# Kernel optimization log

Measured on AMD Instinct MI355X. Metric: run time of the kernel, lower is better.

The kernel has to match this reference:

```python
import jax, jax.numpy as jnp
import numpy as np

N, E, D = 50000, 1200000, 64
NEG_SLOPE = 0.2  # PyG GATConv LeakyReLU slope
EPS_SM = 1e-16   # PyG softmax eps
EPS_LN = 1e-5


def _glorot(key, shape):
    fan = shape[0]
    return jax.random.normal(key, shape, jnp.float32) / np.float32(np.sqrt(fan))


def setup_inputs() -> dict:
    key = jax.random.key(0)
    ks = jax.random.split(key, 16)
    inp = {
        "x": jax.random.normal(ks[0], (N, D), jnp.float32),
        "edge_index": jax.random.randint(ks[1], (2, E), 0, N, dtype=jnp.int32),
        # layer 0: bipartite-style (-1,-1) GATConv -> separate src/dst projections
        "W_src0": _glorot(ks[2], (D, D)), "W_dst0": _glorot(ks[3], (D, D)),
        "a_src0": _glorot(ks[4], (D,)), "a_dst0": _glorot(ks[5], (D,)),
        "b0": jnp.zeros((D,), jnp.float32),
        "lin_W0": _glorot(ks[6], (D, D)), "lin_b0": jnp.zeros((D,), jnp.float32),
        # layers 1,2: int in_channels -> shared projection for src and dst
        "W1": _glorot(ks[7], (D, D)),
        "a_src1": _glorot(ks[8], (D,)), "a_dst1": _glorot(ks[9], (D,)),
        "b1": jnp.zeros((D,), jnp.float32),
        "lin_W1": _glorot(ks[10], (D, D)), "lin_b1": jnp.zeros((D,), jnp.float32),
        "W2": _glorot(ks[11], (D, D)),
        "a_src2": _glorot(ks[12], (D,)), "a_dst2": _glorot(ks[13], (D,)),
        "b2": jnp.zeros((D,), jnp.float32),
        "lin_W2": _glorot(ks[14], (D, D)), "lin_b2": jnp.zeros((D,), jnp.float32),
        "ln_w": jnp.ones((D,), jnp.float32), "ln_b": jnp.zeros((D,), jnp.float32),
        "proj_W": _glorot(ks[15], (D, 1)), "proj_b": jnp.zeros((1,), jnp.float32),
    }
    return inp


def _gat(x_src, x_dst, a_src, a_dst, bias, src, dst):
    # per-edge attention logit: a_src.x_j + a_dst.x_i, LeakyReLU
    alpha = (x_src * a_src).sum(-1)[src] + (x_dst * a_dst).sum(-1)[dst]  # [E]
    alpha = jnp.where(alpha >= 0, alpha, NEG_SLOPE * alpha)
    # segment softmax over edges sharing a destination node
    m = jax.ops.segment_max(alpha, dst, num_segments=N)
    m = jnp.where(jnp.isfinite(m), m, 0.0)  # empty segments -> -inf -> 0
    e = jnp.exp(alpha - m[dst])
    denom = jax.ops.segment_sum(e, dst, num_segments=N)
    w = e / (denom[dst] + EPS_SM)
    # weighted scatter-add aggregation
    return jax.ops.segment_sum(w[:, None] * x_src[src], dst, num_segments=N) + bias


def reference(x, edge_index,
              W_src0, W_dst0, a_src0, a_dst0, b0, lin_W0, lin_b0,
              W1, a_src1, a_dst1, b1, lin_W1, lin_b1,
              W2, a_src2, a_dst2, b2, lin_W2, lin_b2,
              ln_w, ln_b, proj_W, proj_b):
    src, dst = edge_index[0], edge_index[1]
    h = _gat(x @ W_src0, x @ W_dst0, a_src0, a_dst0, b0, src, dst) + x @ lin_W0 + lin_b0
    h = jax.nn.relu(h)
    hp = h @ W1
    h = _gat(hp, hp, a_src1, a_dst1, b1, src, dst) + h @ lin_W1 + lin_b1
    h = jax.nn.relu(h)
    hp = h @ W2
    h = _gat(hp, hp, a_src2, a_dst2, b2, src, dst) + h @ lin_W2 + lin_b2
    # PyG LayerNorm mode='graph': normalize over all nodes and channels
    mu = h.mean()
    var = h.var()
    h = (h - mu) * jax.lax.rsqrt(var + EPS_LN) * ln_w + ln_b
    return h @ proj_W + proj_b  # [N, 1]
```

## Files before the change

kernel.cpp:

```cpp
#include <hip/hip_runtime.h>
#include <hip/hip_bf16.h>

#define NN 50000
#define NE 1200000
#define D 64
#define NEG_SLOPE 0.2f
#define EPS_SM 1e-16f
#define EPS_LN 1e-5f
#define KMAX 4
#define BSH 6
#define NBUK 782
#define BCAP 2048
#define BCAPSH 11
#define EPB 4096
#define NPB 293
#define GEMM_BLOCKS 3125
#define GAT_BLOCKS 12500

typedef __attribute__((ext_vector_type(8))) short short8;
typedef __attribute__((ext_vector_type(4))) float float4v;

__device__ __forceinline__ float waveReduceSum(float v) {
    #pragma unroll
    for (int off = 32; off > 0; off >>= 1)
        v += __shfl_xor(v, off, 64);
    return v;
}
__device__ __forceinline__ float waveReduceMax(float v) {
    #pragma unroll
    for (int off = 32; off > 0; off >>= 1)
        v = fmaxf(v, __shfl_xor(v, off, 64));
    return v;
}
__device__ __forceinline__ float bflo(unsigned v) { return __uint_as_float(v << 16); }
__device__ __forceinline__ float bfhi(unsigned v) { return __uint_as_float(v & 0xffff0000u); }
__device__ __forceinline__ short f2bf_bits(float f) {
    __hip_bfloat16 b = __float2bfloat16(f);
    short v; __builtin_memcpy(&v, &b, 2);
    return v;
}

__global__ void pack_w(const float* __restrict__ W0,
                       const float* __restrict__ W1m,
                       const float* __restrict__ W2m,
                       unsigned short* __restrict__ wpk, int nmats) {
    const int n = nmats * 4096;
    for (int idx = blockIdx.x * 256 + threadIdx.x; idx < n; idx += gridDim.x * 256) {
        const int j = idx & 7;
        const int lane = (idx >> 3) & 63;
        const int khtile = idx >> 9;
        const int kh = khtile & 1;
        const int tile = khtile >> 1;
        const int mat = tile >> 2;
        const int ch = (tile & 3) * 16 + (lane & 15);
        const int k = kh * 32 + (lane >> 4) * 8 + j;
        const float* W = (mat == 0) ? W0 : (mat == 1 ? W1m : W2m);
        wpk[idx] = (unsigned short)f2bf_bits(W[k * D + ch]);
    }
}

template <int NMATS>
__global__ __launch_bounds__(256) void gemm_mfma(
                          const float* __restrict__ hin,
                          const unsigned short* __restrict__ wpk,
                          const float* __restrict__ avs,
                          const float* __restrict__ avd,
                          const float* __restrict__ bgat,
                          const float* __restrict__ blin,
                          __hip_bfloat16* __restrict__ hp,
                          float* __restrict__ agg,
                          float* __restrict__ alpha_s,
                          float* __restrict__ alpha_d) {
    constexpr int NT   = NMATS * 4;
    constexpr int NTPW = NT / 4;
    __shared__ float xt[16 * D];
    __shared__ float ared[2][4][16];

    const int t   = threadIdx.x;
    const int nb0 = blockIdx.x * 16;
    ((float4*)xt)[t] = ((const float4*)(hin + (size_t)nb0 * D))[t];
    __syncthreads();

    const int w    = t >> 6;
    const int lane = t & 63;
    const int mrow = lane & 15;
    const int kq   = lane >> 4;

    short8 a[2];
    #pragma unroll
    for (int kh = 0; kh < 2; ++kh) {
        const float* xp = xt + mrow * D + kh * 32 + kq * 8;
        const float4 f0 = *(const float4*)(xp);
        const float4 f1 = *(const float4*)(xp + 4);
        a[kh][0] = f2bf_bits(f0.x); a[kh][1] = f2bf_bits(f0.y);
        a[kh][2] = f2bf_bits(f0.z); a[kh][3] = f2bf_bits(f0.w);
        a[kh][4] = f2bf_bits(f1.x); a[kh][5] = f2bf_bits(f1.y);
        a[kh][6] = f2bf_bits(f1.z); a[kh][7] = f2bf_bits(f1.w);
    }

    float4v acc[NTPW];
    #pragma unroll
    for (int i = 0; i < NTPW; ++i) {
        const int tile = w * NTPW + i;
        const short8 b0 = *(const short8*)(wpk + ((size_t)(tile * 2 + 0) * 64 + lane) * 8);
        const short8 b1 = *(const short8*)(wpk + ((size_t)(tile * 2 + 1) * 64 + lane) * 8);
        float4v c = {0.f, 0.f, 0.f, 0.f};
        c = __builtin_amdgcn_mfma_f32_16x16x32_bf16(a[0], b0, c, 0, 0, 0);
        c = __builtin_amdgcn_mfma_f32_16x16x32_bf16(a[1], b1, c, 0, 0, 0);
        acc[i] = c;
    }

    float psr[4] = {0.f, 0.f, 0.f, 0.f};
    float pdr[4] = {0.f, 0.f, 0.f, 0.f};
    #pragma unroll
    for (int i = 0; i < NTPW; ++i) {
        const int tile = w * NTPW + i;
        const int mat  = tile >> 2;
        const int c64  = (tile & 3) * 16 + mrow;
        const float av_s = avs[c64], av_d = avd[c64];
        const float bias = blin[c64] + bgat[c64];
        #pragma unroll
        for (int r = 0; r < 4; ++r) {
            const int node = nb0 + kq * 4 + r;
            const float v = acc[i][r];
            if (mat == 0) {
                hp[(size_t)node * D + c64] = __float2bfloat16(v);
                psr[r] += v * av_s;
                if (NMATS == 2) pdr[r] += v * av_d;
            } else if (NMATS == 3 && mat == 1) {
                pdr[r] += v * av_d;
            } else {
                agg[(size_t)node * D + c64] = v + bias;
            }
        }
    }
    #pragma unroll
    for (int off = 1; off < 16; off <<= 1) {
        #pragma unroll
        for (int r = 0; r < 4; ++r) {
            psr[r] += __shfl_xor(psr[r], off, 64);
            pdr[r] += __shfl_xor(pdr[r], off, 64);
        }
    }
    if (mrow == 0) {
        #pragma unroll
        for (int r = 0; r < 4; ++r) {
            ared[0][w][kq * 4 + r] = psr[r];
            ared[1][w][kq * 4 + r] = pdr[r];
        }
    }
    __syncthreads();
    if (t < 16) {
        alpha_s[nb0 + t] = ared[0][0][t] + ared[0][1][t] + ared[0][2][t] + ared[0][3][t];
        alpha_d[nb0 + t] = ared[1][0][t] + ared[1][1][t] + ared[1][2][t] + ared[1][3][t];
    }
}

__global__ __launch_bounds__(256) void bucket_partition(const int* __restrict__ ei,
                                                        int* __restrict__ bcur,
                                                        int* __restrict__ pairs) {
    __shared__ int h[NBUK];
    __shared__ int cur[NBUK];
    for (int i = threadIdx.x; i < NBUK; i += 256) h[i] = 0;
    __syncthreads();
    const int base = blockIdx.x * EPB;
    const int lim  = min(EPB, NE - base);
    for (int i = threadIdx.x; i < lim; i += 256)
        atomicAdd(&h[ei[NE + base + i] >> BSH], 1);
    __syncthreads();
    for (int i = threadIdx.x; i < NBUK; i += 256) {
        const int c = h[i];
        cur[i] = c ? atomicAdd(&bcur[i], c) : 0;
    }
    __syncthreads();
    for (int i = threadIdx.x; i < lim; i += 256) {
        const int s = ei[base + i];
        const int d = ei[NE + base + i];
        const int b = d >> BSH;
        const int pos = atomicAdd(&cur[b], 1);
        if (pos < BCAP) pairs[(b << BCAPSH) + pos] = s | ((d & 63) << 16);
    }
}

__global__ __launch_bounds__(256) void csr_finalize(const int* __restrict__ pairs,
                                                    const int* __restrict__ bcur,
                                                    int* __restrict__ cnt,
                                                    int* __restrict__ row_start,
                                                    int* __restrict__ csr_src) {
    __shared__ int ncnt[64];
    __shared__ int lsrc[BCAP];
    const int t = threadIdx.x;
    const int b = blockIdx.x;
    const int beg = b << BCAPSH;
    const int m = min(bcur[b], BCAP);
    const int nbase = b << BSH;
    if (t < 64) ncnt[t] = 0;
    __syncthreads();
    for (int i = t; i < m; i += 256)
        atomicAdd(&ncnt[pairs[beg + i] >> 16], 1);
    __syncthreads();
    if (t < 64) {
        const int v = ncnt[t];
        int inc = v;
        #pragma unroll
        for (int off = 1; off < 64; off <<= 1) {
            const int u = __shfl_up(inc, off, 64);
            if (t >= off) inc += u;
        }
        const int excl = inc - v;
        if (nbase + t < NN) {
            cnt[nbase + t] = v;
            row_start[nbase + t] = beg + excl;
        }
        ncnt[t] = excl;
    }
    __syncthreads();
    for (int i = t; i < m; i += 256) {
        const int p = pairs[beg + i];
        const int pos = atomicAdd(&ncnt[p >> 16], 1);
        lsrc[pos] = p & 0xffff;
    }
    __syncthreads();
    for (int i = t; i < m; i += 256)
        csr_src[beg + i] = lsrc[i];
}

template <bool DO_RELU, bool DO_STATS>
__global__ __launch_bounds__(256) void gat_node(
                         const int* __restrict__ csr_src,
                         const int* __restrict__ row_start,
                         const int* __restrict__ cnt,
                         const float* __restrict__ as,
                         const float* __restrict__ ad,
                         const __hip_bfloat16* __restrict__ hp,
                         float* __restrict__ agg,
                         float* __restrict__ partial) {
    __shared__ int2 esm[4][KMAX * 64];
    const int wv   = threadIdx.x >> 6;
    const int lane = threadIdx.x & 63;
    const int node = blockIdx.x * 4 + wv;
    const int snode = __builtin_amdgcn_readfirstlane(node);
    const int deg = cnt[snode];
    const int rs  = row_start[snode];
    const int half = lane >> 5;
    const int c2   = lane & 31;
    float2 acc = make_float2(0.f, 0.f);
    if (deg > 0) {
        const float ad_d = ad[snode];
        int   sr[KMAX];
        float ea[KMAX];
        float mx = -INFINITY;
        #pragma unroll
        for (int k = 0; k < KMAX; ++k) {
            const int j = k * 64 + lane;
            const bool valid = j < deg;
            const int s = valid ? __builtin_nontemporal_load(csr_src + rs + j) : 0;
            float a = valid ? (as[s] + ad_d) : -INFINITY;
            a = (a >= 0.f) ? a : NEG_SLOPE * a;
            sr[k] = s;
            ea[k] = a;
            mx = fmaxf(mx, a);
        }
        mx = waveReduceMax(mx);
        float sum = 0.f;
        #pragma unroll
        for (int k = 0; k < KMAX; ++k) {
            float e = __expf(ea[k] - mx);
            e = (k * 64 + lane < deg) ? e : 0.f;
            ea[k] = e;
            sum += e;
        }
        sum = waveReduceSum(sum);
        const float inv = 1.f / (sum + EPS_SM);
        #pragma unroll
        for (int k = 0; k < KMAX; ++k) {
            if (k * 64 < deg)
                esm[wv][k * 64 + lane] = make_int2(sr[k] * 32, __float_as_int(ea[k] * inv));
        }
        const unsigned* hp32 = (const unsigned*)hp;
        const int jmax = (deg + 1) & ~1;
        float2 a0 = make_float2(0.f, 0.f), a1 = make_float2(0.f, 0.f);
        int j = 0;
        for (; j + 4 <= jmax; j += 4) {
            const int2 p0 = esm[wv][j + 0 + half];
            const int2 p1 = esm[wv][j + 2 + half];
            const unsigned v0 = hp32[p0.x + c2];
            const unsigned v1 = hp32[p1.x + c2];
            const float w0 = __int_as_float(p0.y), w1 = __int_as_float(p1.y);
            a0.x = fmaf(w0, bflo(v0), a0.x);
            a0.y = fmaf(w0, bfhi(v0), a0.y);
            a1.x = fmaf(w1, bflo(v1), a1.x);
            a1.y = fmaf(w1, bfhi(v1), a1.y);
        }
        for (; j < jmax; j += 2) {
            const int2 p = esm[wv][j + half];
            const unsigned v = hp32[p.x + c2];
            const float w = __int_as_float(p.y);
            a0.x = fmaf(w, bflo(v), a0.x);
            a0.y = fmaf(w, bfhi(v), a0.y);
        }
        acc.x = a0.x + a1.x;
        acc.y = a0.y + a1.y;
    }
    acc.x += __shfl_xor(acc.x, 32, 64);
    acc.y += __shfl_xor(acc.y, 32, 64);

    float2 r2 = make_float2(0.f, 0.f);
    if (half == 0) {
        const float2 g = *(const float2*)(agg + (size_t)node * D + 2 * c2);
        r2.x = g.x + acc.x;
        r2.y = g.y + acc.y;
        if (DO_RELU) { r2.x = fmaxf(r2.x, 0.f); r2.y = fmaxf(r2.y, 0.f); }
        *(float2*)(agg + (size_t)node * D + 2 * c2) = r2;
    }
    if (DO_STATS) {
        float s  = r2.x + r2.y;
        float ss = r2.x * r2.x + r2.y * r2.y;
        s  = waveReduceSum(s);
        ss = waveReduceSum(ss);
        __shared__ float red[2][4];
        if (lane == 0) { red[0][wv] = s; red[1][wv] = ss; }
        __syncthreads();
        if (threadIdx.x == 0) {
            partial[blockIdx.x]              = red[0][0] + red[0][1] + red[0][2] + red[0][3];
            partial[GAT_BLOCKS + blockIdx.x] = red[1][0] + red[1][1] + red[1][2] + red[1][3];
        }
    }
}

__global__ void ln_reduce(const float* __restrict__ partial, float* __restrict__ stats) {
    float s = 0.f, ss = 0.f;
    for (int i = threadIdx.x; i < GAT_BLOCKS; i += 256) {
        s  += partial[i];
        ss += partial[GAT_BLOCKS + i];
    }
    s  = waveReduceSum(s);
    ss = waveReduceSum(ss);
    __shared__ float sm[2][4];
    if ((threadIdx.x & 63) == 0) {
        sm[0][threadIdx.x >> 6] = s;
        sm[1][threadIdx.x >> 6] = ss;
    }
    __syncthreads();
    if (threadIdx.x == 0) {
        stats[0] = sm[0][0] + sm[0][1] + sm[0][2] + sm[0][3];
        stats[1] = sm[1][0] + sm[1][1] + sm[1][2] + sm[1][3];
    }
}

__global__ void finalize(const float* __restrict__ x,
                         const float* __restrict__ stats,
                         const float* __restrict__ lnw,
                         const float* __restrict__ lnb,
                         const float* __restrict__ pw,
                         const float* __restrict__ pb,
                         float* __restrict__ out) {
    const int wave = (blockIdx.x * blockDim.x + threadIdx.x) >> 6;
    const int lane = threadIdx.x & 63;
    if (wave >= NN) return;
    const float inv_nd = 1.f / (float)(NN * D);
    const float mu  = stats[0] * inv_nd;
    const float var = stats[1] * inv_nd - mu * mu;
    const float rs = rsqrtf(var + EPS_LN);
    const float v = x[(size_t)wave * D + lane];
    const float xn = (v - mu) * rs * lnw[lane] + lnb[lane];
    const float c = waveReduceSum(xn * pw[lane]);
    if (lane == 0) out[wave] = c + pb[0];
}

extern "C" void kernel_launch(void* const* d_in, const int* in_sizes, int n_in,
                              void* d_out, int out_size, void* d_ws, size_t ws_size,
                              hipStream_t stream) {
    const float* x     = (const float*)d_in[0];
    const int*   ei    = (const int*)d_in[1];
    const float* Wsrc0 = (const float*)d_in[2];
    const float* Wdst0 = (const float*)d_in[3];
    const float* asrc0 = (const float*)d_in[4];
    const float* adst0 = (const float*)d_in[5];
    const float* b0    = (const float*)d_in[6];
    const float* linW0 = (const float*)d_in[7];
    const float* linb0 = (const float*)d_in[8];
    const float* W1    = (const float*)d_in[9];
    const float* asrc1 = (const float*)d_in[10];
    const float* adst1 = (const float*)d_in[11];
    const float* b1    = (const float*)d_in[12];
    const float* linW1 = (const float*)d_in[13];
    const float* linb1 = (const float*)d_in[14];
    const float* W2    = (const float*)d_in[15];
    const float* asrc2 = (const float*)d_in[16];
    const float* adst2 = (const float*)d_in[17];
    const float* b2    = (const float*)d_in[18];
    const float* linW2 = (const float*)d_in[19];
    const float* linb2 = (const float*)d_in[20];
    const float* lnw   = (const float*)d_in[21];
    const float* lnb   = (const float*)d_in[22];
    const float* pW    = (const float*)d_in[23];
    const float* pb    = (const float*)d_in[24];
    float* out = (float*)d_out;

    int*  csr_src   = (int*)d_ws;
    int*  cnt       = csr_src + NBUK * BCAP;
    int*  row_start = cnt + NN;
    int*  bcur      = row_start + NN;
    size_t off = (size_t)(NBUK * BCAP + 2 * NN + NBUK);
    off = (off + 3) & ~(size_t)3;
    float* A     = (float*)d_ws + off;
    int*   pairs = (int*)A;
    float* B     = A + (size_t)NN * D;
    __hip_bfloat16* P = (__hip_bfloat16*)(B + NN * D);
    float* alpha_s = (float*)(P + NN * D);
    float* alpha_d = alpha_s + NN;
    float* stats   = alpha_d + NN;
    float* partial = stats + 2;
    unsigned short* wpk = (unsigned short*)(((uintptr_t)(partial + 2 * GAT_BLOCKS) + 15) & ~(uintptr_t)15);

    const int elem_blocks = (NN * D) / 256;

    hipMemsetAsync(bcur, 0, NBUK * sizeof(int), stream);
    bucket_partition<<<NPB, 256, 0, stream>>>(ei, bcur, pairs);
    csr_finalize<<<NBUK, 256, 0, stream>>>(pairs, bcur, cnt, row_start, csr_src);

    pack_w<<<48, 256, 0, stream>>>(Wsrc0, Wdst0, linW0, wpk, 3);
    gemm_mfma<3><<<GEMM_BLOCKS, 256, 0, stream>>>(x, wpk, asrc0, adst0, b0, linb0,
                                                  P, A, alpha_s, alpha_d);
    gat_node<true, false><<<GAT_BLOCKS, 256, 0, stream>>>(csr_src, row_start, cnt,
                                                          alpha_s, alpha_d, P, A, partial);

    pack_w<<<32, 256, 0, stream>>>(W1, linW1, linW1, wpk, 2);
    gemm_mfma<2><<<GEMM_BLOCKS, 256, 0, stream>>>(A, wpk, asrc1, adst1, b1, linb1,
                                                  P, B, alpha_s, alpha_d);
    gat_node<true, false><<<GAT_BLOCKS, 256, 0, stream>>>(csr_src, row_start, cnt,
                                                          alpha_s, alpha_d, P, B, partial);

    pack_w<<<32, 256, 0, stream>>>(W2, linW2, linW2, wpk, 2);
    gemm_mfma<2><<<GEMM_BLOCKS, 256, 0, stream>>>(B, wpk, asrc2, adst2, b2, linb2,
                                                  P, A, alpha_s, alpha_d);
    gat_node<false, true><<<GAT_BLOCKS, 256, 0, stream>>>(csr_src, row_start, cnt,
                                                          alpha_s, alpha_d, P, A, partial);

    ln_reduce<<<1, 256, 0, stream>>>(partial, stats);
    finalize<<<elem_blocks, 256, 0, stream>>>(A, stats, lnw, lnb, pW, pb, out);
}
```

Baseline: 336.9 us.

## Use single-pass unnormalized softmax aggregation in GAT and batch weight packing

The GAT node kernel now computes exp(alpha) and accumulates weighted features and the denominator in one pass over edges, dropping the max-subtraction, the shared-memory staging and the KMAX degree cap. Each 16-lane group handles one edge and loads 4 bf16 channels per lane, and cross-group shuffles reduce the result. All seven weight matrices are packed in one launch at the start rather than three per-layer pack launches. Skipping the max subtraction risks overflow or precision loss for large logits, but removes a reduction and the staging pass.

```diff
diff --git a/kernel.cpp b/kernel.cpp
--- a/kernel.cpp
+++ b/kernel.cpp
@@ -7,7 +7,6 @@
 #define NEG_SLOPE 0.2f
 #define EPS_SM 1e-16f
 #define EPS_LN 1e-5f
-#define KMAX 4
 #define BSH 6
 #define NBUK 782
 #define BCAP 2048
@@ -26,12 +25,6 @@
         v += __shfl_xor(v, off, 64);
     return v;
 }
-__device__ __forceinline__ float waveReduceMax(float v) {
-    #pragma unroll
-    for (int off = 32; off > 0; off >>= 1)
-        v = fmaxf(v, __shfl_xor(v, off, 64));
-    return v;
-}
 __device__ __forceinline__ float bflo(unsigned v) { return __uint_as_float(v << 16); }
 __device__ __forceinline__ float bfhi(unsigned v) { return __uint_as_float(v & 0xffff0000u); }
 __device__ __forceinline__ short f2bf_bits(float f) {
@@ -40,11 +33,10 @@
     return v;
 }
 
-__global__ void pack_w(const float* __restrict__ W0,
-                       const float* __restrict__ W1m,
-                       const float* __restrict__ W2m,
-                       unsigned short* __restrict__ wpk, int nmats) {
-    const int n = nmats * 4096;
+struct WP7 { const float* p[7]; };
+
+__global__ __launch_bounds__(256) void pack_w7(WP7 wp, unsigned short* __restrict__ wpk) {
+    const int n = 7 * 4096;
     for (int idx = blockIdx.x * 256 + threadIdx.x; idx < n; idx += gridDim.x * 256) {
         const int j = idx & 7;
         const int lane = (idx >> 3) & 63;
@@ -54,8 +46,7 @@
         const int mat = tile >> 2;
         const int ch = (tile & 3) * 16 + (lane & 15);
         const int k = kh * 32 + (lane >> 4) * 8 + j;
-        const float* W = (mat == 0) ? W0 : (mat == 1 ? W1m : W2m);
-        wpk[idx] = (unsigned short)f2bf_bits(W[k * D + ch]);
+        wpk[idx] = (unsigned short)f2bf_bits(wp.p[mat][k * D + ch]);
     }
 }
 
@@ -235,91 +226,67 @@
                          const __hip_bfloat16* __restrict__ hp,
                          float* __restrict__ agg,
                          float* __restrict__ partial) {
-    __shared__ int2 esm[4][KMAX * 64];
     const int wv   = threadIdx.x >> 6;
     const int lane = threadIdx.x & 63;
     const int node = blockIdx.x * 4 + wv;
     const int snode = __builtin_amdgcn_readfirstlane(node);
     const int deg = cnt[snode];
     const int rs  = row_start[snode];
-    const int half = lane >> 5;
-    const int c2   = lane & 31;
-    float2 acc = make_float2(0.f, 0.f);
-    if (deg > 0) {
-        const float ad_d = ad[snode];
-        int   sr[KMAX];
-        float ea[KMAX];
-        float mx = -INFINITY;
-        #pragma unroll
-        for (int k = 0; k < KMAX; ++k) {
-            const int j = k * 64 + lane;
-            const bool valid = j < deg;
-            const int s = valid ? __builtin_nontemporal_load(csr_src + rs + j) : 0;
-            float a = valid ? (as[s] + ad_d) : -INFINITY;
-            a = (a >= 0.f) ? a : NEG_SLOPE * a;
-            sr[k] = s;
-            ea[k] = a;
-            mx = fmaxf(mx, a);
-        }
-        mx = waveReduceMax(mx);
-        float sum = 0.f;
-        #pragma unroll
-        for (int k = 0; k < KMAX; ++k) {
-            float e = __expf(ea[k] - mx);
-            e = (k * 64 + lane < deg) ? e : 0.f;
-            ea[k] = e;
-            sum += e;
-        }
-        sum = waveReduceSum(sum);
-        const float inv = 1.f / (sum + EPS_SM);
-        #pragma unroll
-        for (int k = 0; k < KMAX; ++k) {
-            if (k * 64 < deg)
-                esm[wv][k * 64 + lane] = make_int2(sr[k] * 32, __float_as_int(ea[k] * inv));
-        }
-        const unsigned* hp32 = (const unsigned*)hp;
-        const int jmax = (deg + 1) & ~1;
-        float2 a0 = make_float2(0.f, 0.f), a1 = make_float2(0.f, 0.f);
-        int j = 0;
-        for (; j + 4 <= jmax; j += 4) {
-            const int2 p0 = esm[wv][j + 0 + half];
-            const int2 p1 = esm[wv][j + 2 + half];
-            const unsigned v0 = hp32[p0.x + c2];
-            const unsigned v1 = hp32[p1.x + c2];
-            const float w0 = __int_as_float(p0.y), w1 = __int_as_float(p1.y);
-            a0.x = fmaf(w0, bflo(v0), a0.x);
-            a0.y = fmaf(w0, bfhi(v0), a0.y);
-            a1.x = fmaf(w1, bflo(v1), a1.x);
-            a1.y = fmaf(w1, bfhi(v1), a1.y);
-        }
-        for (; j < jmax; j += 2) {
-            const int2 p = esm[wv][j + half];
-            const unsigned v = hp32[p.x + c2];
-            const float w = __int_as_float(p.y);
-            a0.x = fmaf(w, bflo(v), a0.x);
-            a0.y = fmaf(w, bfhi(v), a0.y);
-        }
-        acc.x = a0.x + a1.x;
-        acc.y = a0.y + a1.y;
-    }
-    acc.x += __shfl_xor(acc.x, 32, 64);
-    acc.y += __shfl_xor(acc.y, 32, 64);
-
-    float2 r2 = make_float2(0.f, 0.f);
-    if (half == 0) {
-        const float2 g = *(const float2*)(agg + (size_t)node * D + 2 * c2);
-        r2.x = g.x + acc.x;
-        r2.y = g.y + acc.y;
-        if (DO_RELU) { r2.x = fmaxf(r2.x, 0.f); r2.y = fmaxf(r2.y, 0.f); }
-        *(float2*)(agg + (size_t)node * D + 2 * c2) = r2;
+    const int g   = lane >> 4;
+    const int cl  = lane & 15;
+    const float ad_d = ad[snode];
+    const uint2* hpv = (const uint2*)hp;
+
+    float ax = 0.f, ay = 0.f, az = 0.f, aw = 0.f;
+    float se = 0.f;
+    #pragma unroll 2
+    for (int jb = 0; jb < deg; jb += 4) {
+        const int j = jb + g;
+        const bool valid = j < deg;
+        const int s = valid ? __builtin_nontemporal_load(csr_src + rs + j) : 0;
+        const uint2 v = hpv[(size_t)s * 16 + cl];
+        float a = as[s] + ad_d;
+        a = (a >= 0.f) ? a : NEG_SLOPE * a;
+        const float e = valid ? __expf(a) : 0.f;
+        ax = fmaf(e, bflo(v.x), ax);
+        ay = fmaf(e, bfhi(v.x), ay);
+        az = fmaf(e, bflo(v.y), az);
+        aw = fmaf(e, bfhi(v.y), aw);
+        se += e;
+    }
+    #pragma unroll
+    for (int off = 16; off < 64; off <<= 1) {
+        ax += __shfl_xor(ax, off, 64);
+        ay += __shfl_xor(ay, off, 64);
+        az += __shfl_xor(az, off, 64);
+        aw += __shfl_xor(aw, off, 64);
+        se += __shfl_xor(se, off, 64);
+    }
+    const float inv = 1.f / (se + EPS_SM);
+
+    float s1 = 0.f, s2 = 0.f;
+    if (lane < 16) {
+        const float4 gv = *(const float4*)(agg + (size_t)node * D + 4 * lane);
+        float rx = fmaf(ax, inv, gv.x);
+        float ry = fmaf(ay, inv, gv.y);
+        float rz = fmaf(az, inv, gv.z);
+        float rw = fmaf(aw, inv, gv.w);
+        if (DO_RELU) {
+            rx = fmaxf(rx, 0.f); ry = fmaxf(ry, 0.f);
+            rz = fmaxf(rz, 0.f); rw = fmaxf(rw, 0.f);
+        }
+        const float4 rv = {rx, ry, rz, rw};
+        *(float4*)(agg + (size_t)node * D + 4 * lane) = rv;
+        if (DO_STATS) {
+            s1 = rx + ry + rz + rw;
+            s2 = rx * rx + ry * ry + rz * rz + rw * rw;
+        }
     }
     if (DO_STATS) {
-        float s  = r2.x + r2.y;
-        float ss = r2.x * r2.x + r2.y * r2.y;
-        s  = waveReduceSum(s);
-        ss = waveReduceSum(ss);
+        s1 = waveReduceSum(s1);
+        s2 = waveReduceSum(s2);
         __shared__ float red[2][4];
-        if (lane == 0) { red[0][wv] = s; red[1][wv] = ss; }
+        if (lane == 0) { red[0][wv] = s1; red[1][wv] = s2; }
         __syncthreads();
         if (threadIdx.x == 0) {
             partial[blockIdx.x]              = red[0][0] + red[0][1] + red[0][2] + red[0][3];
@@ -416,24 +383,23 @@
 
     const int elem_blocks = (NN * D) / 256;
 
+    WP7 wp = {{Wsrc0, Wdst0, linW0, W1, linW1, W2, linW2}};
+    pack_w7<<<112, 256, 0, stream>>>(wp, wpk);
     hipMemsetAsync(bcur, 0, NBUK * sizeof(int), stream);
     bucket_partition<<<NPB, 256, 0, stream>>>(ei, bcur, pairs);
     csr_finalize<<<NBUK, 256, 0, stream>>>(pairs, bcur, cnt, row_start, csr_src);
 
-    pack_w<<<48, 256, 0, stream>>>(Wsrc0, Wdst0, linW0, wpk, 3);
     gemm_mfma<3><<<GEMM_BLOCKS, 256, 0, stream>>>(x, wpk, asrc0, adst0, b0, linb0,
                                                   P, A, alpha_s, alpha_d);
     gat_node<true, false><<<GAT_BLOCKS, 256, 0, stream>>>(csr_src, row_start, cnt,
                                                           alpha_s, alpha_d, P, A, partial);
 
-    pack_w<<<32, 256, 0, stream>>>(W1, linW1, linW1, wpk, 2);
-    gemm_mfma<2><<<GEMM_BLOCKS, 256, 0, stream>>>(A, wpk, asrc1, adst1, b1, linb1,
+    gemm_mfma<2><<<GEMM_BLOCKS, 256, 0, stream>>>(A, wpk + 3 * 4096, asrc1, adst1, b1, linb1,
                                                   P, B, alpha_s, alpha_d);
     gat_node<true, false><<<GAT_BLOCKS, 256, 0, stream>>>(csr_src, row_start, cnt,
                                                           alpha_s, alpha_d, P, B, partial);
 
-    pack_w<<<32, 256, 0, stream>>>(W2, linW2, linW2, wpk, 2);
-    gemm_mfma<2><<<GEMM_BLOCKS, 256, 0, stream>>>(B, wpk, asrc2, adst2, b2, linb2,
+    gemm_mfma<2><<<GEMM_BLOCKS, 256, 0, stream>>>(B, wpk + 5 * 4096, asrc2, adst2, b2, linb2,
                                                   P, A, alpha_s, alpha_d);
     gat_node<false, true><<<GAT_BLOCKS, 256, 0, stream>>>(csr_src, row_start, cnt,
                                                           alpha_s, alpha_d, P, A, partial);
```

After: 386.1 us. 14.6% more time.
